# Kernel optimization log

Hardware: AMD Instinct MI355X
Metric: run time of the kernel (lower is better)

## Reference

```python
import jax, jax.numpy as jnp
import numpy as np

VOCAB = 16000
DIM = 1024
B, T = 4, 2048


def setup_inputs() -> dict:
    key = jax.random.key(0)
    k_ids, k_emb, k_w, k_lw, k_lb = jax.random.split(key, 5)
    input_ids = jax.random.randint(k_ids, (B, T), 0, VOCAB)
    embed = jax.random.normal(k_emb, (VOCAB, DIM), dtype=jnp.float32)
    # w_state = I + 0.05 * (default Linear init ~ U(-1/sqrt(dim), 1/sqrt(dim)))
    bound = 1.0 / np.sqrt(DIM)
    w_state = jnp.eye(DIM, dtype=jnp.float32) + 0.05 * jax.random.uniform(
        k_w, (DIM, DIM), minval=-bound, maxval=bound, dtype=jnp.float32)
    lm_w = jax.random.uniform(k_lw, (VOCAB, DIM), minval=-bound, maxval=bound, dtype=jnp.float32)
    lm_b = jax.random.uniform(k_lb, (VOCAB,), minval=-bound, maxval=bound, dtype=jnp.float32)
    return {"input_ids": input_ids, "embed": embed, "w_state": w_state,
            "lm_w": lm_w, "lm_b": lm_b}


def reference(input_ids, embed, w_state, lm_w, lm_b):
    # h: [B, T, D]
    h = embed[input_ids]
    state0 = jnp.zeros((h.shape[0], h.shape[2]), dtype=h.dtype)

    def step(state, h_t):
        # nn.Linear: state @ W^T ; then add input injection
        new_state = state @ w_state.T + h_t
        return new_state, new_state

    # scan over time: inputs [T, B, D]
    _, outs = jax.lax.scan(step, state0, jnp.swapaxes(h, 0, 1))
    hidden = jnp.swapaxes(outs, 0, 1)  # [B, T, D]
    logits = hidden @ lm_w.T + lm_b    # [B, T, V]
    return logits
```

## Files before the change

kernel.cpp:

```cpp
#include <hip/hip_runtime.h>
#include <hip/hip_bf16.h>
#include <stdint.h>

#define DD 1024
#define BB 4
#define TT 2048
#define VV 16000
#define LCH 8
#define NR 1024
#define PADR 512
#define NPAD 16128
#define M1C ((size_t)DD * DD)

typedef __bf16 bf16_t;
typedef float f32x4_t __attribute__((ext_vector_type(4)));
typedef bf16_t bf16x8_t __attribute__((ext_vector_type(8)));
typedef bf16_t bf16x4_t __attribute__((ext_vector_type(4)));

#define KIND_SQ 0
#define KIND_ROUND 1
#define KIND_LEVEL 2
#define KIND_CARRY 3

__device__ __forceinline__ void gload16(const void* g, void* l) {
  __builtin_amdgcn_global_load_lds((const __attribute__((address_space(1))) void*)g,
                                   (__attribute__((address_space(3))) void*)l, 16, 0, 0);
}

__global__ __launch_bounds__(256) void k_cvt(const float* __restrict__ src,
                                             bf16_t* __restrict__ dst, int n4) {
  int i = blockIdx.x * blockDim.x + threadIdx.x;
  int stride = gridDim.x * blockDim.x;
  for (; i < n4; i += stride) {
    float4 v = ((const float4*)src)[i];
    union { ushort4 u; bf16_t h[4]; } p;
    p.h[0] = (bf16_t)v.x; p.h[1] = (bf16_t)v.y;
    p.h[2] = (bf16_t)v.z; p.h[3] = (bf16_t)v.w;
    ((ushort4*)dst)[i] = p.u;
  }
}

struct JobF {
  const float* A; const float* B; float* C; const float* Cin;
  int kind; int dlt;
};
struct JobsF { JobF j[8]; };

__global__ __launch_bounds__(256) void k_gatherF(const float* __restrict__ embed,
                                                 const int* __restrict__ ids,
                                                 float* __restrict__ slab0) {
  int r = blockIdx.x;
  int b = r & 3, c = r >> 2;
  int id = ids[b * TT + c * LCH];
  const float4* s = (const float4*)(embed + (size_t)id * DD);
  float4* d = (float4*)(slab0 + (size_t)r * DD);
  for (int i = threadIdx.x; i < DD / 4; i += blockDim.x) d[i] = s[i];
}

template <int NS>
__device__ __forceinline__ void swrite(char* base, int byteoff, float4 v) {
  float r0 = v.x, r1 = v.y, r2 = v.z, r3 = v.w;
#pragma unroll
  for (int p = 0; p < NS; ++p) {
    bf16x4_t h;
    h[0] = (bf16_t)r0; h[1] = (bf16_t)r1; h[2] = (bf16_t)r2; h[3] = (bf16_t)r3;
    *(bf16x4_t*)(base + p * 5120 + byteoff) = h;
    if (p + 1 < NS) {
      r0 -= (float)h[0]; r1 -= (float)h[1]; r2 -= (float)h[2]; r3 -= (float)h[3];
    }
  }
}

template <int NS, bool NN, int MODE>
__device__ __forceinline__ void mbodyF(bf16_t* __restrict__ SBb, const JobF& jb,
                                       const float* __restrict__ embed,
                                       const int* __restrict__ ids,
                                       bf16_t* __restrict__ hidden) {
  const float* A = jb.A;
  const float* Bm = jb.B;
  const int tid = threadIdx.x, lane = tid & 63, wave = tid >> 6;
  const int i0 = blockIdx.y * 64, j0 = blockIdx.x * 64;
  const int wm = (wave >> 1) * 32, wn = (wave & 1) * 32;
  char* Ap = (char*)SBb;
  char* Bp = Ap + NS * 5120;
  const int arow = tid >> 2;
  const int akb = (tid & 3) * 8;
  const int bj = tid & 63, bk4 = (tid >> 6) * 4;
  const int frow = lane & 15, fkb = (lane >> 4) * 16;
  f32x4_t acc[2][2] = {};

  const float* Aptr = A + (size_t)(i0 + arow) * DD + (tid & 3) * 4;
  const float* BptrNT = Bm + (size_t)(j0 + arow) * DD + (tid & 3) * 4;
  const float* BptrNN = Bm + (size_t)bk4 * DD + j0 + bj;

  float4 a0 = *(const float4*)(Aptr);
  float4 a1 = *(const float4*)(Aptr + 16);
  float4 b0, b1;
  float s0[4], s1[4];
  if (!NN) {
    b0 = *(const float4*)(BptrNT);
    b1 = *(const float4*)(BptrNT + 16);
  } else {
#pragma unroll
    for (int s = 0; s < 4; ++s) s0[s] = BptrNN[(size_t)s * DD];
#pragma unroll
    for (int s = 0; s < 4; ++s) s1[s] = BptrNN[(size_t)(16 + s) * DD];
  }

  for (int k0 = 0;;) {
    __syncthreads();
    swrite<NS>(Ap, arow * 80 + akb, a0);
    swrite<NS>(Ap, arow * 80 + akb + 32, a1);
    if (!NN) {
      swrite<NS>(Bp, arow * 80 + akb, b0);
      swrite<NS>(Bp, arow * 80 + akb + 32, b1);
    } else {
      float4 t0; t0.x = s0[0]; t0.y = s0[1]; t0.z = s0[2]; t0.w = s0[3];
      float4 t1; t1.x = s1[0]; t1.y = s1[1]; t1.z = s1[2]; t1.w = s1[3];
      swrite<NS>(Bp, bj * 80 + bk4 * 2, t0);
      swrite<NS>(Bp, bj * 80 + bk4 * 2 + 32, t1);
    }
    __syncthreads();
    int kn = k0 + 32;
    if (kn < DD) {
      a0 = *(const float4*)(Aptr + kn);
      a1 = *(const float4*)(Aptr + kn + 16);
      if (!NN) {
        b0 = *(const float4*)(BptrNT + kn);
        b1 = *(const float4*)(BptrNT + kn + 16);
      } else {
#pragma unroll
        for (int s = 0; s < 4; ++s) s0[s] = BptrNN[(size_t)(kn + s) * DD];
#pragma unroll
        for (int s = 0; s < 4; ++s) s1[s] = BptrNN[(size_t)(kn + 16 + s) * DD];
      }
    }
    bf16x8_t af[NS][2], bfx[NS][2];
#pragma unroll
    for (int p = 0; p < NS; ++p)
#pragma unroll
      for (int mf = 0; mf < 2; ++mf) {
        af[p][mf] = *(const bf16x8_t*)(Ap + p * 5120 + (wm + mf * 16 + frow) * 80 + fkb);
        bfx[p][mf] = *(const bf16x8_t*)(Bp + p * 5120 + (wn + mf * 16 + frow) * 80 + fkb);
      }
#pragma unroll
    for (int pa = 0; pa < NS; ++pa)
#pragma unroll
      for (int pb = 0; pb < NS; ++pb) {
        if (pa + pb < NS) {
#pragma unroll
          for (int mf = 0; mf < 2; ++mf)
#pragma unroll
            for (int nf = 0; nf < 2; ++nf)
              acc[mf][nf] = __builtin_amdgcn_mfma_f32_16x16x32_bf16(
                  af[pa][mf], bfx[pb][nf], acc[mf][nf], 0, 0, 0);
        }
      }
    k0 = kn;
    if (k0 >= DD) break;
  }

  const int ecol = lane & 15, er4 = (lane >> 4) * 4;
#pragma unroll
  for (int mf = 0; mf < 2; ++mf) {
#pragma unroll
    for (int nf = 0; nf < 2; ++nf) {
      const int rb = i0 + wm + mf * 16 + er4;
      const int cj = j0 + wn + nf * 16 + ecol;
#pragma unroll
      for (int rg = 0; rg < 4; ++rg) {
        const int ri = rb + rg;
        float v = acc[mf][nf][rg];
        if (MODE == 0) {
          jb.C[(size_t)ri * DD + cj] = v;
        } else if (MODE == 1) {
          int b = ri & 3, c = ri >> 2, t = c * LCH + jb.dlt;
          v += embed[(size_t)ids[b * TT + t] * DD + cj];
          jb.C[(size_t)ri * DD + cj] = v;
        } else if (MODE == 2) {
          v += jb.Cin[(size_t)ri * DD + cj];
          jb.C[(size_t)ri * DD + cj] = v;
        } else {
          int b = ri & 3, c = ri >> 2, t = c * LCH + jb.dlt;
          hidden[((size_t)b * TT + t) * DD + cj] =
              (bf16_t)(v + jb.Cin[(size_t)ri * DD + cj]);
        }
      }
    }
  }
}

__global__ __launch_bounds__(256, 2) void k_multiF(JobsF jobs,
                                                   const float* __restrict__ embed,
                                                   const int* __restrict__ ids,
                                                   bf16_t* __restrict__ hidden) {
  __shared__ __align__(16) bf16_t SBb[6 * 2560];
  const JobF& jb = jobs.j[blockIdx.z];
  if (jb.kind == KIND_SQ)
    mbodyF<3, true, 0>(SBb, jb, embed, ids, hidden);
  else if (jb.kind == KIND_ROUND)
    mbodyF<2, false, 1>(SBb, jb, embed, ids, hidden);
  else if (jb.kind == KIND_LEVEL)
    mbodyF<2, false, 2>(SBb, jb, embed, ids, hidden);
  else
    mbodyF<2, false, 3>(SBb, jb, embed, ids, hidden);
}

#define NTK 32

__global__ __launch_bounds__(512, 2) void k_lmhead2(
    const bf16_t* __restrict__ Ah, const bf16_t* __restrict__ Bw,
    const float* __restrict__ bias, float* __restrict__ Cout) {
  __shared__ __align__(16) char LB[4 * 32768];
  const int tid = threadIdx.x, lane = tid & 63, wave = tid >> 6;
  const int wr = wave >> 2, wc = wave & 3;
  int orig = blockIdx.x * 32 + blockIdx.y;
  int swz = (orig & 7) * 252 + (orig >> 3);
  int bx = swz / 32, by = swz % 32;
  const int m0 = by * 256, n0 = bx * 256;

  const int srow = tid >> 2;
  const int scb = (tid & 3) * 16;

  auto stageA = [&](int t) {
    char* buf = LB + (size_t)(t & 3) * 32768;
#pragma unroll
    for (int p = 0; p < 2; ++p) {
      int row = p * 128 + srow;
      int sw = ((row >> 1) & 3) << 4;
      gload16((const char*)Ah + ((size_t)(m0 + row) * DD + t * 32) * 2 + (scb ^ sw),
              buf + p * 8192 + wave * 1024);
    }
  };
  auto stageB = [&](int t) {
    char* buf = LB + (size_t)(t & 3) * 32768 + 16384;
#pragma unroll
    for (int p = 0; p < 2; ++p) {
      int row = p * 128 + srow;
      int sw = ((row >> 1) & 3) << 4;
      gload16((const char*)Bw + ((size_t)(n0 + row) * DD + t * 32) * 2 + (scb ^ sw),
              buf + p * 8192 + wave * 1024);
    }
  };

  const int frow = lane & 15;
  const int c4b = (lane >> 4) * 16;
  f32x4_t acc[8][4] = {};

  stageA(0); stageB(0); stageA(1); stageB(1); stageA(2); stageB(2);
  asm volatile("s_waitcnt vmcnt(8)\ns_barrier" ::: "memory");

  for (int t = 0; t < NTK; ++t) {
    char* Abuf = LB + (size_t)(t & 3) * 32768;
    char* Bbuf = Abuf + 16384;
    bf16x8_t afr[4], bfr[4];
#pragma unroll
    for (int nf = 0; nf < 4; ++nf) {
      int r = wc * 64 + nf * 16 + frow;
      bfr[nf] = *(const bf16x8_t*)(Bbuf + r * 64 + (c4b ^ (((r >> 1) & 3) << 4)));
    }
#pragma unroll
    for (int mf = 0; mf < 4; ++mf) {
      int r = wr * 128 + mf * 16 + frow;
      afr[mf] = *(const bf16x8_t*)(Abuf + r * 64 + (c4b ^ (((r >> 1) & 3) << 4)));
    }
    if (t + 3 < NTK) stageA(t + 3);
    __builtin_amdgcn_s_barrier();
    __builtin_amdgcn_s_setprio(1);
#pragma unroll
    for (int mf = 0; mf < 4; ++mf)
#pragma unroll
      for (int nf = 0; nf < 4; ++nf)
        acc[mf][nf] = __builtin_amdgcn_mfma_f32_16x16x32_bf16(
            afr[mf], bfr[nf], acc[mf][nf], 0, 0, 0);
    __builtin_amdgcn_s_setprio(0);
    __builtin_amdgcn_s_barrier();
#pragma unroll
    for (int mf = 0; mf < 4; ++mf) {
      int r = wr * 128 + 64 + mf * 16 + frow;
      afr[mf] = *(const bf16x8_t*)(Abuf + r * 64 + (c4b ^ (((r >> 1) & 3) << 4)));
    }
    if (t + 3 < NTK) stageB(t + 3);
    __builtin_amdgcn_s_barrier();
    __builtin_amdgcn_s_setprio(1);
#pragma unroll
    for (int mf = 0; mf < 4; ++mf)
#pragma unroll
      for (int nf = 0; nf < 4; ++nf)
        acc[4 + mf][nf] = __builtin_amdgcn_mfma_f32_16x16x32_bf16(
            afr[mf], bfr[nf], acc[4 + mf][nf], 0, 0, 0);
    __builtin_amdgcn_s_setprio(0);
    if (t < NTK - 3) {
      asm volatile("s_waitcnt vmcnt(8)\ns_barrier" ::: "memory");
    } else if (t == NTK - 3) {
      asm volatile("s_waitcnt vmcnt(4)\ns_barrier" ::: "memory");
    } else if (t == NTK - 2) {
      asm volatile("s_waitcnt vmcnt(0)\ns_barrier" ::: "memory");
    }
  }

  const int ecol = lane & 15, er4 = (lane >> 4) * 4;
#pragma unroll
  for (int mf = 0; mf < 8; ++mf) {
#pragma unroll
    for (int nf = 0; nf < 4; ++nf) {
      int gm = m0 + wr * 128 + mf * 16 + er4;
      int gn = n0 + wc * 64 + nf * 16 + ecol;
      if (gn < VV) {
        float bv = bias[gn];
#pragma unroll
        for (int rg = 0; rg < 4; ++rg)
          Cout[(size_t)(gm + rg) * VV + gn] = acc[mf][nf][rg] + bv;
      }
    }
  }
}

extern "C" void kernel_launch(void* const* d_in, const int* in_sizes, int n_in,
                              void* d_out, int out_size, void* d_ws, size_t ws_size,
                              hipStream_t stream) {
  (void)in_sizes; (void)n_in; (void)out_size; (void)ws_size;
  const int* ids = (const int*)d_in[0];
  const float* embed = (const float*)d_in[1];
  const float* w_state = (const float*)d_in[2];
  const float* lm_w = (const float*)d_in[3];
  const float* lm_b = (const float*)d_in[4];
  float* out = (float*)d_out;

  const size_t M1 = M1C;
  float* PW = (float*)d_ws;
  float* Q = PW + 8 * M1;
  float* LOC = Q + 7 * M1;
  float* E0 = LOC + 8 * M1;
  float* E1 = E0 + (size_t)(PADR + NR) * DD;
  bf16_t* HID = (bf16_t*)(E1 + (size_t)(PADR + NR) * DD);
  bf16_t* LWB = HID + (size_t)BB * TT * DD;
  float* E0d = E0 + (size_t)PADR * DD;
  float* E1d = E1 + (size_t)PADR * DD;

  k_cvt<<<2048, 256, 0, stream>>>(lm_w, LWB, VV * DD / 4);
  hipMemsetAsync(LWB + (size_t)VV * DD, 0,
                 (size_t)(NPAD - VV) * DD * sizeof(bf16_t), stream);
  hipMemcpyAsync(PW, w_state, M1 * sizeof(float), hipMemcpyDeviceToDevice, stream);
  k_gatherF<<<NR, 256, 0, stream>>>(embed, ids, LOC);
  hipMemsetAsync(E0, 0, (size_t)PADR * DD * sizeof(float), stream);
  hipMemsetAsync(E1, 0, (size_t)PADR * DD * sizeof(float), stream);

  JobsF J{};
  J.j[0] = JobF{w_state, w_state, PW + M1, nullptr, KIND_SQ, 0};
  J.j[1] = JobF{LOC, w_state, LOC + M1, nullptr, KIND_ROUND, 1};
  k_multiF<<<dim3(16, 16, 2), 256, 0, stream>>>(J, embed, ids, HID);
  J.j[0] = JobF{PW + M1, w_state, PW + 2 * M1, nullptr, KIND_SQ, 0};
  J.j[1] = JobF{PW + M1, PW + M1, PW + 3 * M1, nullptr, KIND_SQ, 0};
  J.j[2] = JobF{LOC + M1, w_state, LOC + 2 * M1, nullptr, KIND_ROUND, 2};
  k_multiF<<<dim3(16, 16, 3), 256, 0, stream>>>(J, embed, ids, HID);
  J.j[0] = JobF{PW + 3 * M1, w_state, PW + 4 * M1, nullptr, KIND_SQ, 0};
  J.j[1] = JobF{PW + 3 * M1, PW + M1, PW + 5 * M1, nullptr, KIND_SQ, 0};
  J.j[2] = JobF{PW + 3 * M1, PW + 2 * M1, PW + 6 * M1, nullptr, KIND_SQ, 0};
  J.j[3] = JobF{PW + 3 * M1, PW + 3 * M1, PW + 7 * M1, nullptr, KIND_SQ, 0};
  J.j[4] = JobF{LOC + 2 * M1, w_state, LOC + 3 * M1, nullptr, KIND_ROUND, 3};
  k_multiF<<<dim3(16, 16, 5), 256, 0, stream>>>(J, embed, ids, HID);
  for (int d = 4; d <= 7; ++d) {
    const float* src = (d == 4) ? (PW + 7 * M1) : (Q + (size_t)(d - 5) * M1);
    J.j[0] = JobF{src, src, Q + (size_t)(d - 4) * M1, nullptr, KIND_SQ, 0};
    J.j[1] = JobF{LOC + (size_t)(d - 1) * M1, w_state, LOC + (size_t)d * M1,
                  nullptr, KIND_ROUND, d};
    k_multiF<<<dim3(16, 16, 2), 256, 0, stream>>>(J, embed, ids, HID);
  }
  hipMemcpyAsync(E0d, LOC + 7 * M1, M1 * sizeof(float),
                 hipMemcpyDeviceToDevice, stream);

  float* inp = E0d;
  float* outp = E1d;
  for (int k = 0; k < 8; ++k) {
    JobsF J2{};
    int nz = 0;
    if (k <= 2) {
      const float* src = Q + (size_t)(k + 3) * M1;
      J2.j[nz++] = JobF{src, src, Q + (size_t)(k + 4) * M1, nullptr, KIND_SQ, 0};
    }
    const float* Bq = (k == 0) ? (PW + 7 * M1) : (Q + (size_t)(k - 1) * M1);
    J2.j[nz++] = JobF{inp - (size_t)(4 << k) * DD, Bq, outp, inp, KIND_LEVEL, 0};
    k_multiF<<<dim3(16, 16, nz), 256, 0, stream>>>(J2, embed, ids, HID);
    float* t = inp; inp = outp; outp = t;
  }

  JobsF Jc{};
  for (int d = 0; d < 8; ++d)
    Jc.j[d] = JobF{inp - (size_t)4 * DD, PW + (size_t)d * M1, nullptr,
                   LOC + (size_t)d * M1, KIND_CARRY, d};
  k_multiF<<<dim3(16, 16, 8), 256, 0, stream>>>(Jc, embed, ids, HID);

  dim3 gl(NPAD / 256, (BB * TT) / 256);
  k_lmhead2<<<gl, 512, 0, stream>>>(HID, LWB, lm_b, out);
}
```

Baseline: 908.5 us.

## Restructure LM-head GEMM pipeline with register double-buffered LDS fragments

Reworks the LM-head GEMM main loop so each iteration issues all A and B global loads for a stage together. Fragments for the next k-tile are read from LDS into a second register set while the current tile's MFMAs run, with one barrier per tile instead of three. It also changes the block-index swizzle to a row-major traversal over 63 column tiles and makes the logits stores nontemporal. The aim is to hide LDS latency and cut synchronisation stalls, at the cost of more VGPRs, which could spill or reduce occupancy.

```diff
diff --git a/kernel.cpp b/kernel.cpp
--- a/kernel.cpp
+++ b/kernel.cpp
@@ -208,21 +208,21 @@
 
 #define NTK 32
 
-__global__ __launch_bounds__(512, 2) void k_lmhead2(
+__global__ __launch_bounds__(512, 2) void k_lmhead3(
     const bf16_t* __restrict__ Ah, const bf16_t* __restrict__ Bw,
     const float* __restrict__ bias, float* __restrict__ Cout) {
   __shared__ __align__(16) char LB[4 * 32768];
   const int tid = threadIdx.x, lane = tid & 63, wave = tid >> 6;
   const int wr = wave >> 2, wc = wave & 3;
-  int orig = blockIdx.x * 32 + blockIdx.y;
+  int orig = blockIdx.y * gridDim.x + blockIdx.x;
   int swz = (orig & 7) * 252 + (orig >> 3);
-  int bx = swz / 32, by = swz % 32;
+  int by = swz / 63, bx = swz % 63;
   const int m0 = by * 256, n0 = bx * 256;
 
   const int srow = tid >> 2;
   const int scb = (tid & 3) * 16;
 
-  auto stageA = [&](int t) {
+  auto stage = [&](int t) {
     char* buf = LB + (size_t)(t & 3) * 32768;
 #pragma unroll
     for (int p = 0; p < 2; ++p) {
@@ -230,16 +230,8 @@
       int sw = ((row >> 1) & 3) << 4;
       gload16((const char*)Ah + ((size_t)(m0 + row) * DD + t * 32) * 2 + (scb ^ sw),
               buf + p * 8192 + wave * 1024);
-    }
-  };
-  auto stageB = [&](int t) {
-    char* buf = LB + (size_t)(t & 3) * 32768 + 16384;
-#pragma unroll
-    for (int p = 0; p < 2; ++p) {
-      int row = p * 128 + srow;
-      int sw = ((row >> 1) & 3) << 4;
       gload16((const char*)Bw + ((size_t)(n0 + row) * DD + t * 32) * 2 + (scb ^ sw),
-              buf + p * 8192 + wave * 1024);
+              buf + 16384 + p * 8192 + wave * 1024);
     }
   };
 
@@ -247,56 +239,75 @@
   const int c4b = (lane >> 4) * 16;
   f32x4_t acc[8][4] = {};
 
-  stageA(0); stageB(0); stageA(1); stageB(1); stageA(2); stageB(2);
-  asm volatile("s_waitcnt vmcnt(8)\ns_barrier" ::: "memory");
-
-  for (int t = 0; t < NTK; ++t) {
-    char* Abuf = LB + (size_t)(t & 3) * 32768;
-    char* Bbuf = Abuf + 16384;
-    bf16x8_t afr[4], bfr[4];
+  stage(0); stage(1); stage(2);
+  asm volatile("s_waitcnt vmcnt(4)\ns_barrier" ::: "memory");
+
+  bf16x8_t sB0[4], sA0[4], sB1[4], sA1[4];
+  {
+    char* Abuf = LB;
+    char* Bbuf = LB + 16384;
 #pragma unroll
     for (int nf = 0; nf < 4; ++nf) {
       int r = wc * 64 + nf * 16 + frow;
-      bfr[nf] = *(const bf16x8_t*)(Bbuf + r * 64 + (c4b ^ (((r >> 1) & 3) << 4)));
+      sB0[nf] = *(const bf16x8_t*)(Bbuf + r * 64 + (c4b ^ (((r >> 1) & 3) << 4)));
     }
 #pragma unroll
     for (int mf = 0; mf < 4; ++mf) {
       int r = wr * 128 + mf * 16 + frow;
-      afr[mf] = *(const bf16x8_t*)(Abuf + r * 64 + (c4b ^ (((r >> 1) & 3) << 4)));
-    }
-    if (t + 3 < NTK) stageA(t + 3);
-    __builtin_amdgcn_s_barrier();
+      sA0[mf] = *(const bf16x8_t*)(Abuf + r * 64 + (c4b ^ (((r >> 1) & 3) << 4)));
+    }
+  }
+
+  auto tile = [&](int t, bf16x8_t (&PB)[4], bf16x8_t (&PA1)[4],
+                  bf16x8_t (&NB)[4], bf16x8_t (&NA1)[4]) {
+    char* Abuf = LB + (size_t)(t & 3) * 32768;
+    char* AbufN = LB + (size_t)((t + 1) & 3) * 32768;
+    char* BbufN = AbufN + 16384;
+    bf16x8_t rA2[4];
+#pragma unroll
+    for (int mf = 0; mf < 4; ++mf) {
+      int r = wr * 128 + 64 + mf * 16 + frow;
+      rA2[mf] = *(const bf16x8_t*)(Abuf + r * 64 + (c4b ^ (((r >> 1) & 3) << 4)));
+    }
+    if (t + 1 < NTK) {
+#pragma unroll
+      for (int nf = 0; nf < 4; ++nf) {
+        int r = wc * 64 + nf * 16 + frow;
+        NB[nf] = *(const bf16x8_t*)(BbufN + r * 64 + (c4b ^ (((r >> 1) & 3) << 4)));
+      }
+#pragma unroll
+      for (int mf = 0; mf < 4; ++mf) {
+        int r = wr * 128 + mf * 16 + frow;
+        NA1[mf] = *(const bf16x8_t*)(AbufN + r * 64 + (c4b ^ (((r >> 1) & 3) << 4)));
+      }
+    }
+    if (t + 3 < NTK) stage(t + 3);
     __builtin_amdgcn_s_setprio(1);
 #pragma unroll
     for (int mf = 0; mf < 4; ++mf)
 #pragma unroll
       for (int nf = 0; nf < 4; ++nf)
         acc[mf][nf] = __builtin_amdgcn_mfma_f32_16x16x32_bf16(
-            afr[mf], bfr[nf], acc[mf][nf], 0, 0, 0);
-    __builtin_amdgcn_s_setprio(0);
-    __builtin_amdgcn_s_barrier();
-#pragma unroll
-    for (int mf = 0; mf < 4; ++mf) {
-      int r = wr * 128 + 64 + mf * 16 + frow;
-      afr[mf] = *(const bf16x8_t*)(Abuf + r * 64 + (c4b ^ (((r >> 1) & 3) << 4)));
-    }
-    if (t + 3 < NTK) stageB(t + 3);
-    __builtin_amdgcn_s_barrier();
-    __builtin_amdgcn_s_setprio(1);
+            PA1[mf], PB[nf], acc[mf][nf], 0, 0, 0);
 #pragma unroll
     for (int mf = 0; mf < 4; ++mf)
 #pragma unroll
       for (int nf = 0; nf < 4; ++nf)
         acc[4 + mf][nf] = __builtin_amdgcn_mfma_f32_16x16x32_bf16(
-            afr[mf], bfr[nf], acc[4 + mf][nf], 0, 0, 0);
+            rA2[mf], PB[nf], acc[4 + mf][nf], 0, 0, 0);
     __builtin_amdgcn_s_setprio(0);
     if (t < NTK - 3) {
-      asm volatile("s_waitcnt vmcnt(8)\ns_barrier" ::: "memory");
+      asm volatile("s_waitcnt vmcnt(4)\ns_barrier" ::: "memory");
     } else if (t == NTK - 3) {
-      asm volatile("s_waitcnt vmcnt(4)\ns_barrier" ::: "memory");
-    } else if (t == NTK - 2) {
       asm volatile("s_waitcnt vmcnt(0)\ns_barrier" ::: "memory");
-    }
+    } else if (t < NTK - 1) {
+      __builtin_amdgcn_s_barrier();
+    }
+  };
+
+  for (int t = 0; t < NTK; t += 2) {
+    tile(t, sB0, sA0, sB1, sA1);
+    tile(t + 1, sB1, sA1, sB0, sA0);
   }
 
   const int ecol = lane & 15, er4 = (lane >> 4) * 4;
@@ -310,7 +321,8 @@
         float bv = bias[gn];
 #pragma unroll
         for (int rg = 0; rg < 4; ++rg)
-          Cout[(size_t)(gm + rg) * VV + gn] = acc[mf][nf][rg] + bv;
+          __builtin_nontemporal_store(acc[mf][nf][rg] + bv,
+                                      &Cout[(size_t)(gm + rg) * VV + gn]);
       }
     }
   }
@@ -392,5 +404,5 @@
   k_multiF<<<dim3(16, 16, 8), 256, 0, stream>>>(Jc, embed, ids, HID);
 
   dim3 gl(NPAD / 256, (BB * TT) / 256);
-  k_lmhead2<<<gl, 512, 0, stream>>>(HID, LWB, lm_b, out);
-}
+  k_lmhead3<<<gl, 512, 0, stream>>>(HID, LWB, lm_b, out);
+}
```

Result: no change. 916.3 us (+0.9%).

## Double-buffer LDS in recurrence GEMM and merge LM-head staging with fewer barriers

Applied to the files above, without the earlier changes.

The multi-job fp32-split GEMM now uses two LDS buffers and two register sets, so global loads and LDS staging for the next K tile overlap compute on the current one. This removes one barrier per iteration at the cost of doubling shared memory, which may reduce occupancy. The LM-head kernel issues its A and B tile loads together at the top of each iteration and drops the intra-iteration barriers. Its block-index swizzle is also changed to map row-major over the grid.

```diff
diff --git a/kernel.cpp b/kernel.cpp
--- a/kernel.cpp
+++ b/kernel.cpp
@@ -72,7 +72,7 @@
 }
 
 template <int NS, bool NN, int MODE>
-__device__ __forceinline__ void mbodyF(bf16_t* __restrict__ SBb, const JobF& jb,
+__device__ __forceinline__ void mbodyF(bf16_t* __restrict__ SBall, const JobF& jb,
                                        const float* __restrict__ embed,
                                        const int* __restrict__ ids,
                                        bf16_t* __restrict__ hidden) {
@@ -81,8 +81,8 @@
   const int tid = threadIdx.x, lane = tid & 63, wave = tid >> 6;
   const int i0 = blockIdx.y * 64, j0 = blockIdx.x * 64;
   const int wm = (wave >> 1) * 32, wn = (wave & 1) * 32;
-  char* Ap = (char*)SBb;
-  char* Bp = Ap + NS * 5120;
+  char* base0 = (char*)SBall;
+  char* base1 = base0 + NS * 2 * 5120;
   const int arow = tid >> 2;
   const int akb = (tid & 3) * 8;
   const int bj = tid & 63, bk4 = (tid >> 6) * 4;
@@ -93,48 +93,39 @@
   const float* BptrNT = Bm + (size_t)(j0 + arow) * DD + (tid & 3) * 4;
   const float* BptrNN = Bm + (size_t)bk4 * DD + j0 + bj;
 
-  float4 a0 = *(const float4*)(Aptr);
-  float4 a1 = *(const float4*)(Aptr + 16);
-  float4 b0, b1;
-  float s0[4], s1[4];
-  if (!NN) {
-    b0 = *(const float4*)(BptrNT);
-    b1 = *(const float4*)(BptrNT + 16);
-  } else {
-#pragma unroll
-    for (int s = 0; s < 4; ++s) s0[s] = BptrNN[(size_t)s * DD];
-#pragma unroll
-    for (int s = 0; s < 4; ++s) s1[s] = BptrNN[(size_t)(16 + s) * DD];
-  }
-
-  for (int k0 = 0;;) {
-    __syncthreads();
-    swrite<NS>(Ap, arow * 80 + akb, a0);
-    swrite<NS>(Ap, arow * 80 + akb + 32, a1);
+  struct Regs { float4 a0, a1, b0, b1; float s0[4], s1[4]; };
+
+  auto gload = [&](Regs& R, int k0) {
+    R.a0 = *(const float4*)(Aptr + k0);
+    R.a1 = *(const float4*)(Aptr + k0 + 16);
     if (!NN) {
-      swrite<NS>(Bp, arow * 80 + akb, b0);
-      swrite<NS>(Bp, arow * 80 + akb + 32, b1);
+      R.b0 = *(const float4*)(BptrNT + k0);
+      R.b1 = *(const float4*)(BptrNT + k0 + 16);
     } else {
-      float4 t0; t0.x = s0[0]; t0.y = s0[1]; t0.z = s0[2]; t0.w = s0[3];
-      float4 t1; t1.x = s1[0]; t1.y = s1[1]; t1.z = s1[2]; t1.w = s1[3];
+#pragma unroll
+      for (int s = 0; s < 4; ++s) R.s0[s] = BptrNN[(size_t)(k0 + s) * DD];
+#pragma unroll
+      for (int s = 0; s < 4; ++s) R.s1[s] = BptrNN[(size_t)(k0 + 16 + s) * DD];
+    }
+  };
+  auto stage = [&](Regs& R, char* buf) {
+    char* Ap = buf;
+    char* Bp = buf + NS * 5120;
+    swrite<NS>(Ap, arow * 80 + akb, R.a0);
+    swrite<NS>(Ap, arow * 80 + akb + 32, R.a1);
+    if (!NN) {
+      swrite<NS>(Bp, arow * 80 + akb, R.b0);
+      swrite<NS>(Bp, arow * 80 + akb + 32, R.b1);
+    } else {
+      float4 t0; t0.x = R.s0[0]; t0.y = R.s0[1]; t0.z = R.s0[2]; t0.w = R.s0[3];
+      float4 t1; t1.x = R.s1[0]; t1.y = R.s1[1]; t1.z = R.s1[2]; t1.w = R.s1[3];
       swrite<NS>(Bp, bj * 80 + bk4 * 2, t0);
       swrite<NS>(Bp, bj * 80 + bk4 * 2 + 32, t1);
     }
-    __syncthreads();
-    int kn = k0 + 32;
-    if (kn < DD) {
-      a0 = *(const float4*)(Aptr + kn);
-      a1 = *(const float4*)(Aptr + kn + 16);
-      if (!NN) {
-        b0 = *(const float4*)(BptrNT + kn);
-        b1 = *(const float4*)(BptrNT + kn + 16);
-      } else {
-#pragma unroll
-        for (int s = 0; s < 4; ++s) s0[s] = BptrNN[(size_t)(kn + s) * DD];
-#pragma unroll
-        for (int s = 0; s < 4; ++s) s1[s] = BptrNN[(size_t)(kn + 16 + s) * DD];
-      }
-    }
+  };
+  auto compute = [&](char* buf) {
+    char* Ap = buf;
+    char* Bp = buf + NS * 5120;
     bf16x8_t af[NS][2], bfx[NS][2];
 #pragma unroll
     for (int p = 0; p < NS; ++p)
@@ -156,8 +147,22 @@
                   af[pa][mf], bfx[pb][nf], acc[mf][nf], 0, 0, 0);
         }
       }
-    k0 = kn;
-    if (k0 >= DD) break;
+  };
+
+  Regs R0, R1;
+  gload(R0, 0);
+  gload(R1, 32);
+  stage(R0, base0);
+  __syncthreads();
+  for (int kt = 0; kt < 32; kt += 2) {
+    stage(R1, base1);
+    if (kt + 2 < 32) gload(R0, (kt + 2) * 32);
+    compute(base0);
+    __syncthreads();
+    if (kt + 2 < 32) stage(R0, base0);
+    if (kt + 3 < 32) gload(R1, (kt + 3) * 32);
+    compute(base1);
+    __syncthreads();
   }
 
   const int ecol = lane & 15, er4 = (lane >> 4) * 4;
@@ -194,7 +199,7 @@
                                                    const float* __restrict__ embed,
                                                    const int* __restrict__ ids,
                                                    bf16_t* __restrict__ hidden) {
-  __shared__ __align__(16) bf16_t SBb[6 * 2560];
+  __shared__ __align__(16) bf16_t SBb[2 * 6 * 2560];
   const JobF& jb = jobs.j[blockIdx.z];
   if (jb.kind == KIND_SQ)
     mbodyF<3, true, 0>(SBb, jb, embed, ids, hidden);
@@ -214,15 +219,15 @@
   __shared__ __align__(16) char LB[4 * 32768];
   const int tid = threadIdx.x, lane = tid & 63, wave = tid >> 6;
   const int wr = wave >> 2, wc = wave & 3;
-  int orig = blockIdx.x * 32 + blockIdx.y;
+  int orig = blockIdx.y * gridDim.x + blockIdx.x;
   int swz = (orig & 7) * 252 + (orig >> 3);
-  int bx = swz / 32, by = swz % 32;
+  int by = swz / 63, bx = swz % 63;
   const int m0 = by * 256, n0 = bx * 256;
 
   const int srow = tid >> 2;
   const int scb = (tid & 3) * 16;
 
-  auto stageA = [&](int t) {
+  auto stage = [&](int t) {
     char* buf = LB + (size_t)(t & 3) * 32768;
 #pragma unroll
     for (int p = 0; p < 2; ++p) {
@@ -230,16 +235,8 @@
       int sw = ((row >> 1) & 3) << 4;
       gload16((const char*)Ah + ((size_t)(m0 + row) * DD + t * 32) * 2 + (scb ^ sw),
               buf + p * 8192 + wave * 1024);
-    }
-  };
-  auto stageB = [&](int t) {
-    char* buf = LB + (size_t)(t & 3) * 32768 + 16384;
-#pragma unroll
-    for (int p = 0; p < 2; ++p) {
-      int row = p * 128 + srow;
-      int sw = ((row >> 1) & 3) << 4;
       gload16((const char*)Bw + ((size_t)(n0 + row) * DD + t * 32) * 2 + (scb ^ sw),
-              buf + p * 8192 + wave * 1024);
+              buf + 16384 + p * 8192 + wave * 1024);
     }
   };
 
@@ -247,12 +244,13 @@
   const int c4b = (lane >> 4) * 16;
   f32x4_t acc[8][4] = {};
 
-  stageA(0); stageB(0); stageA(1); stageB(1); stageA(2); stageB(2);
+  stage(0); stage(1); stage(2);
   asm volatile("s_waitcnt vmcnt(8)\ns_barrier" ::: "memory");
 
   for (int t = 0; t < NTK; ++t) {
     char* Abuf = LB + (size_t)(t & 3) * 32768;
     char* Bbuf = Abuf + 16384;
+    if (t + 3 < NTK) stage(t + 3);
     bf16x8_t afr[4], bfr[4];
 #pragma unroll
     for (int nf = 0; nf < 4; ++nf) {
@@ -264,8 +262,6 @@
       int r = wr * 128 + mf * 16 + frow;
       afr[mf] = *(const bf16x8_t*)(Abuf + r * 64 + (c4b ^ (((r >> 1) & 3) << 4)));
     }
-    if (t + 3 < NTK) stageA(t + 3);
-    __builtin_amdgcn_s_barrier();
     __builtin_amdgcn_s_setprio(1);
 #pragma unroll
     for (int mf = 0; mf < 4; ++mf)
@@ -274,14 +270,11 @@
         acc[mf][nf] = __builtin_amdgcn_mfma_f32_16x16x32_bf16(
             afr[mf], bfr[nf], acc[mf][nf], 0, 0, 0);
     __builtin_amdgcn_s_setprio(0);
-    __builtin_amdgcn_s_barrier();
 #pragma unroll
     for (int mf = 0; mf < 4; ++mf) {
       int r = wr * 128 + 64 + mf * 16 + frow;
       afr[mf] = *(const bf16x8_t*)(Abuf + r * 64 + (c4b ^ (((r >> 1) & 3) << 4)));
     }
-    if (t + 3 < NTK) stageB(t + 3);
-    __builtin_amdgcn_s_barrier();
     __builtin_amdgcn_s_setprio(1);
 #pragma unroll
     for (int mf = 0; mf < 4; ++mf)
```

Measured after the change: 952.3 us. 4.8% more time.

## Shrink LM-head tile to 128x256 with double-buffered LDS for higher occupancy

Applied to the files above, without the earlier changes.

The LM-head GEMM kernel now uses 128x256 output tiles instead of 256x256, with a two-stage LDS buffer (48KB) instead of four stages (128KB). Launch bounds go up to 4 blocks per CU and the grid doubles in the M dimension, with a swizzle remapped for 63x64 blocks. The goal is more resident waves and less register pressure, so latency is hidden by occupancy rather than deep prefetch. The cost is lower arithmetic intensity per tile, more global and L2 traffic for B, and a shallower prefetch pipeline.

```diff
diff --git a/kernel.cpp b/kernel.cpp
--- a/kernel.cpp
+++ b/kernel.cpp
@@ -208,51 +208,46 @@
 
 #define NTK 32
 
-__global__ __launch_bounds__(512, 2) void k_lmhead2(
+__global__ __launch_bounds__(512, 4) void k_lmhead4(
     const bf16_t* __restrict__ Ah, const bf16_t* __restrict__ Bw,
     const float* __restrict__ bias, float* __restrict__ Cout) {
-  __shared__ __align__(16) char LB[4 * 32768];
+  __shared__ __align__(16) char LB[2 * 24576];
   const int tid = threadIdx.x, lane = tid & 63, wave = tid >> 6;
   const int wr = wave >> 2, wc = wave & 3;
-  int orig = blockIdx.x * 32 + blockIdx.y;
-  int swz = (orig & 7) * 252 + (orig >> 3);
-  int bx = swz / 32, by = swz % 32;
-  const int m0 = by * 256, n0 = bx * 256;
-
-  const int srow = tid >> 2;
-  const int scb = (tid & 3) * 16;
-
-  auto stageA = [&](int t) {
-    char* buf = LB + (size_t)(t & 3) * 32768;
+  int orig = blockIdx.y * gridDim.x + blockIdx.x;
+  int swz = (orig & 7) * 504 + (orig >> 3);
+  int by = swz / 63, bx = swz % 63;
+  const int m0 = by * 128, n0 = bx * 256;
+
+  auto stage = [&](int t) {
+    char* buf = LB + (size_t)(t & 1) * 24576;
+    {
+      int tpos = tid * 16;
+      int row = tpos >> 6;
+      int scol = (tpos & 63) ^ (((row >> 1) & 3) << 4);
+      gload16((const char*)Ah + ((size_t)(m0 + row) * DD + t * 32) * 2 + scol,
+              buf + wave * 1024);
+    }
 #pragma unroll
     for (int p = 0; p < 2; ++p) {
-      int row = p * 128 + srow;
-      int sw = ((row >> 1) & 3) << 4;
-      gload16((const char*)Ah + ((size_t)(m0 + row) * DD + t * 32) * 2 + (scb ^ sw),
-              buf + p * 8192 + wave * 1024);
-    }
-  };
-  auto stageB = [&](int t) {
-    char* buf = LB + (size_t)(t & 3) * 32768 + 16384;
-#pragma unroll
-    for (int p = 0; p < 2; ++p) {
-      int row = p * 128 + srow;
-      int sw = ((row >> 1) & 3) << 4;
-      gload16((const char*)Bw + ((size_t)(n0 + row) * DD + t * 32) * 2 + (scb ^ sw),
-              buf + p * 8192 + wave * 1024);
+      int tpos = p * 8192 + tid * 16;
+      int row = tpos >> 6;
+      int scol = (tpos & 63) ^ (((row >> 1) & 3) << 4);
+      gload16((const char*)Bw + ((size_t)(n0 + row) * DD + t * 32) * 2 + scol,
+              buf + 8192 + p * 8192 + wave * 1024);
     }
   };
 
   const int frow = lane & 15;
   const int c4b = (lane >> 4) * 16;
-  f32x4_t acc[8][4] = {};
-
-  stageA(0); stageB(0); stageA(1); stageB(1); stageA(2); stageB(2);
-  asm volatile("s_waitcnt vmcnt(8)\ns_barrier" ::: "memory");
+  f32x4_t acc[4][4] = {};
+
+  stage(0); stage(1);
+  asm volatile("s_waitcnt vmcnt(3)\ns_barrier" ::: "memory");
 
   for (int t = 0; t < NTK; ++t) {
-    char* Abuf = LB + (size_t)(t & 3) * 32768;
-    char* Bbuf = Abuf + 16384;
+    char* Abuf = LB + (size_t)(t & 1) * 24576;
+    char* Bbuf = Abuf + 8192;
     bf16x8_t afr[4], bfr[4];
 #pragma unroll
     for (int nf = 0; nf < 4; ++nf) {
@@ -261,11 +256,12 @@
     }
 #pragma unroll
     for (int mf = 0; mf < 4; ++mf) {
-      int r = wr * 128 + mf * 16 + frow;
+      int r = wr * 64 + mf * 16 + frow;
       afr[mf] = *(const bf16x8_t*)(Abuf + r * 64 + (c4b ^ (((r >> 1) & 3) << 4)));
     }
-    if (t + 3 < NTK) stageA(t + 3);
-    __builtin_amdgcn_s_barrier();
+    asm volatile("s_waitcnt lgkmcnt(0)\ns_barrier" ::: "memory");
+    __builtin_amdgcn_sched_barrier(0);
+    if (t + 2 < NTK) stage(t + 2);
     __builtin_amdgcn_s_setprio(1);
 #pragma unroll
     for (int mf = 0; mf < 4; ++mf)
@@ -274,26 +270,8 @@
         acc[mf][nf] = __builtin_amdgcn_mfma_f32_16x16x32_bf16(
             afr[mf], bfr[nf], acc[mf][nf], 0, 0, 0);
     __builtin_amdgcn_s_setprio(0);
-    __builtin_amdgcn_s_barrier();
-#pragma unroll
-    for (int mf = 0; mf < 4; ++mf) {
-      int r = wr * 128 + 64 + mf * 16 + frow;
-      afr[mf] = *(const bf16x8_t*)(Abuf + r * 64 + (c4b ^ (((r >> 1) & 3) << 4)));
-    }
-    if (t + 3 < NTK) stageB(t + 3);
-    __builtin_amdgcn_s_barrier();
-    __builtin_amdgcn_s_setprio(1);
-#pragma unroll
-    for (int mf = 0; mf < 4; ++mf)
-#pragma unroll
-      for (int nf = 0; nf < 4; ++nf)
-        acc[4 + mf][nf] = __builtin_amdgcn_mfma_f32_16x16x32_bf16(
-            afr[mf], bfr[nf], acc[4 + mf][nf], 0, 0, 0);
-    __builtin_amdgcn_s_setprio(0);
-    if (t < NTK - 3) {
-      asm volatile("s_waitcnt vmcnt(8)\ns_barrier" ::: "memory");
-    } else if (t == NTK - 3) {
-      asm volatile("s_waitcnt vmcnt(4)\ns_barrier" ::: "memory");
+    if (t < NTK - 2) {
+      asm volatile("s_waitcnt vmcnt(3)\ns_barrier" ::: "memory");
     } else if (t == NTK - 2) {
       asm volatile("s_waitcnt vmcnt(0)\ns_barrier" ::: "memory");
     }
@@ -301,10 +279,10 @@
 
   const int ecol = lane & 15, er4 = (lane >> 4) * 4;
 #pragma unroll
-  for (int mf = 0; mf < 8; ++mf) {
+  for (int mf = 0; mf < 4; ++mf) {
 #pragma unroll
     for (int nf = 0; nf < 4; ++nf) {
-      int gm = m0 + wr * 128 + mf * 16 + er4;
+      int gm = m0 + wr * 64 + mf * 16 + er4;
       int gn = n0 + wc * 64 + nf * 16 + ecol;
       if (gn < VV) {
         float bv = bias[gn];
@@ -391,6 +369,6 @@
                    LOC + (size_t)d * M1, KIND_CARRY, d};
   k_multiF<<<dim3(16, 16, 8), 256, 0, stream>>>(Jc, embed, ids, HID);
 
-  dim3 gl(NPAD / 256, (BB * TT) / 256);
-  k_lmhead2<<<gl, 512, 0, stream>>>(HID, LWB, lm_b, out);
-}
+  dim3 gl(NPAD / 256, (BB * TT) / 128);
+  k_lmhead4<<<gl, 512, 0, stream>>>(HID, LWB, lm_b, out);
+}
```

Result: slower. 978.7 us (+7.7%).
